# Kernel tuning notes

Hardware: AMD Instinct MI355X
Metric: run time of the kernel (lower is better)

## Reference

```python
import jax, jax.numpy as jnp
import numpy as np

ALPHA = 1.0  # softness coefficient


def _soft_assign(data, centroids):
    # data: (B, N, D), centroids: (B, K, D)
    # squared euclidean distance -> (B, N, K)
    dist = jnp.sum((data[:, :, None, :] - centroids[:, None, :, :]) ** 2, axis=-1)
    return jax.nn.softmax(-ALPHA * dist, axis=2)


def _update_once(data, probs):
    # weighted centroid update: (B, K, D)
    denom = jnp.sum(probs, axis=1)  # (B, K)
    centroids = jnp.einsum('bnk,bnd->bkd', probs, data) / denom[:, :, None]
    probs = _soft_assign(data, centroids)
    return probs, centroids


def setup_inputs() -> dict:
    key = jax.random.key(0)
    k1, k2 = jax.random.split(key)
    B, N, D, K = 8, 65536, 40, 2
    data = jax.random.normal(k1, (B, N, D), dtype=jnp.float32)
    centroid_ids = jax.random.randint(k2, (B, K), 0, N)
    return {"data": data, "centroid_ids": centroid_ids, "iteration": 10}


def reference(data, centroid_ids, iteration):
    # init centroids by gathering selected samples (random init path)
    centroids = jnp.take_along_axis(data, centroid_ids[:, :, None], axis=1)  # (B, K, D)
    probs = _soft_assign(data, centroids)

    def body(i, carry):
        probs, _ = carry
        return _update_once(data, probs)

    probs, centroids = jax.lax.fori_loop(0, iteration, body, (probs, centroids))
    return probs
```

## Files before the change

kernel.cpp:

```cpp
#include <hip/hip_runtime.h>
#include <hip/hip_fp16.h>
#include <cstddef>

#define BB    8
#define NN    65536
#define DD    40
#define NITER 10

#define PREPB  128
#define PTPB   256
#define PTILES 2
#define PSTR   21
#define PBLK   64
#define TPB    256
#define PPT    4
#define ROW    44



__device__ __forceinline__ float rfl(float x) {
    return __int_as_float(__builtin_amdgcn_readfirstlane(__float_as_int(x)));
}
__device__ __forceinline__ float prob0(float diff) {
    return __builtin_amdgcn_rcpf(1.f + __expf(diff));
}
__device__ __forceinline__ float2 h2f(unsigned u) {
    return __half22float2(*(const __half2*)&u);
}

__device__ __forceinline__ void gh_from_ids(const float* __restrict__ data,
                                            const int* __restrict__ ids, int b,
                                            float gs[DD], float& hs, int tid) {
    __shared__ float gbuf[DD], sqbuf[DD], hbuf;
    if (tid < DD) {
        const int i0 = ids[b * 2 + 0];
        const int i1 = ids[b * 2 + 1];
        const float c0 = data[((size_t)b * NN + i0) * DD + tid];
        const float c1 = data[((size_t)b * NN + i1) * DD + tid];
        gbuf[tid]  = c0 - c1;
        sqbuf[tid] = c0 * c0 - c1 * c1;
    }
    __syncthreads();
    if (tid == 0) {
        float h = 0.f;
#pragma unroll
        for (int i = 0; i < DD; ++i) h += sqbuf[i];
        hbuf = h;
    }
    __syncthreads();
#pragma unroll
    for (int i = 0; i < DD; ++i) gs[i] = rfl(gbuf[i]);
    hs = rfl(hbuf);
    __syncthreads();
}

template <int ROWS>
__device__ __forceinline__ void gh_from_partials(const float* __restrict__ pp,
                                                 const float* __restrict__ S, int b,
                                                 float gs[DD], float& hs, int tid) {
    __shared__ float part[41][4];
    __shared__ float red[41], gbuf[DD], sqbuf[DD], hbuf;
    if (tid < 164) {
        const int v = tid % 41, q = tid / 41;
        const float* base = pp + (size_t)b * ROWS * ROW;
        float s = 0.f;
#pragma unroll 8
        for (int j = 0; j < ROWS / 4; ++j)
            s += base[(size_t)(q * (ROWS / 4) + j) * ROW + v];
        part[v][q] = s;
    }
    __syncthreads();
    if (tid < 41)
        red[tid] = (part[tid][0] + part[tid][1]) + (part[tid][2] + part[tid][3]);
    __syncthreads();
    if (tid < DD) {
        const float num = red[tid], den = red[DD];
        const float c0 = num / den;
        const float c1 = (S[b * DD + tid] - num) / ((float)NN - den);
        gbuf[tid]  = c0 - c1;
        sqbuf[tid] = c0 * c0 - c1 * c1;
    }
    __syncthreads();
    if (tid == 0) {
        float h = 0.f;
#pragma unroll
        for (int i = 0; i < DD; ++i) h += sqbuf[i];
        hbuf = h;
    }
    __syncthreads();
#pragma unroll
    for (int i = 0; i < DD; ++i) gs[i] = rfl(gbuf[i]);
    hs = rfl(hbuf);
    __syncthreads();
}


__global__ __launch_bounds__(PTPB, 3) void k_prep(const float* __restrict__ data,
                                                  const int* __restrict__ ids,
                                                  __half2* __restrict__ dataT,
                                                  float* __restrict__ psOut,
                                                  float* __restrict__ ppOut) {
    const int bid = blockIdx.x;
    const int b = bid & 7, pb = bid >> 3;
    const int tid = threadIdx.x;
    __shared__ unsigned stg[PTPB * PSTR];
    __half2* stgh = (__half2*)stg;

    float gs[DD], hs;
    gh_from_ids(data, ids, b, gs, hs, tid);

    float vals[2 * DD + 1];
#pragma unroll
    for (int i = 0; i <= 2 * DD; ++i) vals[i] = 0.f;

#pragma unroll
    for (int t = 0; t < PTILES; ++t) {
        const int basePt = pb * (PTPB * PTILES) + t * PTPB;
        const float4* src = (const float4*)(data + ((size_t)b * NN + basePt) * DD);
        __syncthreads();
#pragma unroll
        for (int j = 0; j < 10; ++j) {
            const unsigned f = tid + j * PTPB;
            const float4 v = src[f];
            const unsigned slot = (f / 10u) * PSTR + (f % 10u) * 2u;
            stgh[slot]     = __floats2half2_rn(v.x, v.y);
            stgh[slot + 1] = __floats2half2_rn(v.z, v.w);
        }
        __syncthreads();
        __half2 xh[20];
        const __half2* rp = stgh + tid * PSTR;
#pragma unroll
        for (int q = 0; q < 20; ++q) xh[q] = rp[q];

        __half2* dst = dataT + (size_t)b * (DD / 2) * NN + basePt + tid;
#pragma unroll
        for (int q = 0; q < 20; ++q) dst[(size_t)q * NN] = xh[q];

        float a0 = 0.f, a1 = 0.f, a2 = 0.f, a3 = 0.f;
#pragma unroll
        for (int q = 0; q < 20; ++q) {
            const float2 v = __half22float2(xh[q]);
            vals[41 + 2 * q] += v.x; vals[41 + 2 * q + 1] += v.y;
            if (q & 1) { a2 = fmaf(v.x, gs[2 * q], a2); a3 = fmaf(v.y, gs[2 * q + 1], a3); }
            else       { a0 = fmaf(v.x, gs[2 * q], a0); a1 = fmaf(v.y, gs[2 * q + 1], a1); }
        }
        const float p0 = prob0(fmaf(-2.f, (a0 + a1) + (a2 + a3), hs));
        vals[DD] += p0;
#pragma unroll
        for (int q = 0; q < 20; ++q) {
            const float2 v = __half22float2(xh[q]);
            vals[2 * q]     = fmaf(p0, v.x, vals[2 * q]);
            vals[2 * q + 1] = fmaf(p0, v.y, vals[2 * q + 1]);
        }
    }

#pragma unroll
    for (int i = 0; i <= 2 * DD; ++i) {
        vals[i] += __shfl_xor(vals[i], 32, 64);
        vals[i] += __shfl_xor(vals[i], 16, 64);
    }
    float* rbuf = (float*)stg;
    __shared__ float part2[2 * DD + 1][2];
    __syncthreads();
    const int lane = tid & 63, wave = tid >> 6;
    if (lane < 16) {
        const int row = wave * 16 + lane;
#pragma unroll
        for (int i = 0; i <= 2 * DD; ++i) rbuf[row * 84 + i] = vals[i];
    }
    __syncthreads();
    if (tid < 162) {
        const int v = tid % 81, q = tid / 81;
        float s = 0.f;
#pragma unroll 8
        for (int j = 0; j < 32; ++j) s += rbuf[(q * 32 + j) * 84 + v];
        part2[v][q] = s;
    }
    __syncthreads();
    if (tid < 81) {
        const float s = part2[tid][0] + part2[tid][1];
        if (tid < 41) ppOut[(size_t)(b * PREPB + pb) * ROW + tid] = s;
        else          psOut[(size_t)(b * PREPB + pb) * 40 + (tid - 41)] = s;
    }
}

__global__ void k_reduceS(const float* __restrict__ psIn, float* __restrict__ S) {
    const int tid = threadIdx.x;
    __shared__ float tmp[BB * DD][2];
    const int i = tid >> 1, half = tid & 1;
    if (i < BB * DD) {
        const int b = i / DD, d = i % DD;
        float s = 0.f;
#pragma unroll 8
        for (int r = 0; r < PREPB / 2; ++r)
            s += psIn[(size_t)(b * PREPB + half * (PREPB / 2) + r) * 40 + d];
        tmp[i][half] = s;
    }
    __syncthreads();
    if (i < BB * DD && half == 0) S[i] = tmp[i][0] + tmp[i][1];
}

template <int MODE, int ROWS>
__global__ __launch_bounds__(TPB, 2) void k_pass(const __half2* __restrict__ dataT,
                                                 const float* __restrict__ ppIn,
                                                 const float* __restrict__ S,
                                                 float* __restrict__ ppOut,
                                                 float* __restrict__ out) {
    const int bid = blockIdx.x;
    const int b = bid & 7, pb = bid >> 3;
    const int tid = threadIdx.x;

    float gs[DD], hs;
    gh_from_partials<ROWS>(ppIn, S, b, gs, hs, tid);

    const int n0 = pb * (TPB * PPT) + tid * PPT;
    const __half2* base = dataT + (size_t)b * (DD / 2) * NN + n0;

    unsigned xh0[20], xh1[20], xh2[20], xh3[20];
    float a00 = 0.f, a01 = 0.f, a10 = 0.f, a11 = 0.f;
    float a20 = 0.f, a21 = 0.f, a30 = 0.f, a31 = 0.f;
#pragma unroll
    for (int dp = 0; dp < DD / 2; ++dp) {
        const uint4 u = *(const uint4*)(base + (size_t)dp * NN);
        xh0[dp] = u.x; xh1[dp] = u.y; xh2[dp] = u.z; xh3[dp] = u.w;
        const float2 v0 = h2f(u.x), v1 = h2f(u.y), v2 = h2f(u.z), v3 = h2f(u.w);
        a00 = fmaf(v0.x, gs[2 * dp], a00); a01 = fmaf(v0.y, gs[2 * dp + 1], a01);
        a10 = fmaf(v1.x, gs[2 * dp], a10); a11 = fmaf(v1.y, gs[2 * dp + 1], a11);
        a20 = fmaf(v2.x, gs[2 * dp], a20); a21 = fmaf(v2.y, gs[2 * dp + 1], a21);
        a30 = fmaf(v3.x, gs[2 * dp], a30); a31 = fmaf(v3.y, gs[2 * dp + 1], a31);
    }
    const float p00 = prob0(fmaf(-2.f, a00 + a01, hs));
    const float p01 = prob0(fmaf(-2.f, a10 + a11, hs));
    const float p02 = prob0(fmaf(-2.f, a20 + a21, hs));
    const float p03 = prob0(fmaf(-2.f, a30 + a31, hs));

    if constexpr (MODE == 2) {
        float4* o = (float4*)(out + ((size_t)b * NN + n0) * 2);
        o[0] = make_float4(p00, 1.f - p00, p01, 1.f - p01);
        o[1] = make_float4(p02, 1.f - p02, p03, 1.f - p03);
    } else {
        float acc[DD + 1];
#pragma unroll
        for (int i = 0; i < DD; ++i) acc[i] = 0.f;
        acc[DD] = (p00 + p01) + (p02 + p03);
#pragma unroll
        for (int dp = 0; dp < DD / 2; ++dp) {
            const float2 v0 = h2f(xh0[dp]), v1 = h2f(xh1[dp]);
            const float2 v2 = h2f(xh2[dp]), v3 = h2f(xh3[dp]);
            acc[2 * dp]     = fmaf(p00, v0.x, fmaf(p01, v1.x,
                              fmaf(p02, v2.x, fmaf(p03, v3.x, acc[2 * dp]))));
            acc[2 * dp + 1] = fmaf(p00, v0.y, fmaf(p01, v1.y,
                              fmaf(p02, v2.y, fmaf(p03, v3.y, acc[2 * dp + 1]))));
        }

#pragma unroll
        for (int i = 0; i <= DD; ++i) {
            acc[i] += __shfl_xor(acc[i], 32, 64);
            acc[i] += __shfl_xor(acc[i], 16, 64);
        }
        __shared__ float rbuf[64 * ROW];
        __shared__ float part2[DD + 1][4];
        const int lane = tid & 63, wave = tid >> 6;
        if (lane < 16) {
            const int row = wave * 16 + lane;
#pragma unroll
            for (int i = 0; i <= DD; ++i) rbuf[row * ROW + i] = acc[i];
        }
        __syncthreads();
        if (tid < 164) {
            const int v = tid % 41, q = tid / 41;
            float s = 0.f;
#pragma unroll
            for (int j = 0; j < 16; ++j) s += rbuf[(q * 16 + j) * ROW + v];
            part2[v][q] = s;
        }
        __syncthreads();
        if (tid <= DD)
            ppOut[(size_t)(b * PBLK + pb) * ROW + tid] =
                (part2[tid][0] + part2[tid][1]) + (part2[tid][2] + part2[tid][3]);
    }
}


extern "C" void kernel_launch(void* const* d_in, const int* in_sizes, int n_in,
                              void* d_out, int out_size, void* d_ws, size_t ws_size,
                              hipStream_t stream) {
    const float* data = (const float*)d_in[0];
    const int*   ids  = (const int*)d_in[1];

    float* ws      = (float*)d_ws;
    __half2* dataT = (__half2*)ws;
    float* after   = ws + (size_t)BB * (DD / 2) * NN;
    float* pA      = after;
    float* pp1     = pA + (size_t)BB * PREPB * ROW;
    float* pp2     = pp1 + (size_t)BB * PBLK * ROW;
    float* pS      = pp2 + (size_t)BB * PBLK * ROW;
    float* S       = pS + (size_t)BB * PREPB * 40;
    float* out     = (float*)d_out;

    k_prep<<<PREPB * BB, PTPB, 0, stream>>>(data, ids, dataT, pS, pA);
    k_reduceS<<<1, 640, 0, stream>>>(pS, S);

    const int grid = PBLK * BB;
    k_pass<1, PREPB><<<grid, TPB, 0, stream>>>(dataT, pA, S, pp1, nullptr);
    const float* cur = pp1;
    float* nxt = pp2;
    for (int t = 0; t < NITER - 2; ++t) {
        k_pass<1, PBLK><<<grid, TPB, 0, stream>>>(dataT, cur, S, nxt, nullptr);
        const float* tmp = cur; cur = nxt; nxt = (float*)tmp;
    }
    k_pass<2, PBLK><<<grid, TPB, 0, stream>>>(dataT, cur, S, nullptr, out);
}
```

Before: 142.3 us.

## Fold column-sum reduction into first pass and prefetch data before centroid reduce

Removes the separate k_reduceS launch by having k_prep write per-block partials that include the per-dimension data sums. The first k_pass reduces these partials and stores S for later passes. Every pass now issues its half-precision data loads before the cross-block partial reduction, so the global load latency overlaps with the centroid computation. The cost is holding the 80 data registers live across the reduction and barriers, which may raise register pressure, and the first pass reads a wider partials buffer.

```diff
diff --git a/kernel.cpp b/kernel.cpp
--- a/kernel.cpp
+++ b/kernel.cpp
@@ -11,11 +11,11 @@
 #define PTPB   256
 #define PTILES 2
 #define PSTR   21
+#define ROW1   84
 #define PBLK   64
 #define TPB    256
 #define PPT    4
 #define ROW    44
-
 
 
 __device__ __forceinline__ float rfl(float x) {
@@ -54,19 +54,58 @@
     __syncthreads();
 }
 
-template <int ROWS>
-__device__ __forceinline__ void gh_from_partials(const float* __restrict__ pp,
-                                                 const float* __restrict__ S, int b,
-                                                 float gs[DD], float& hs, int tid) {
+__device__ __forceinline__ void gh_first(const float* __restrict__ pp,
+                                         float* __restrict__ Sg, int b,
+                                         float gs[DD], float& hs, int tid) {
+    __shared__ float part[81][2];
+    __shared__ float red[81], gbuf[DD], sqbuf[DD], hbuf;
+    if (tid < 162) {
+        const int v = tid % 81, q = tid / 81;
+        const float* base = pp + (size_t)b * PREPB * ROW1;
+        float s = 0.f;
+#pragma unroll 8
+        for (int j = 0; j < 64; ++j)
+            s += base[(size_t)(q * 64 + j) * ROW1 + v];
+        part[v][q] = s;
+    }
+    __syncthreads();
+    if (tid < 81) red[tid] = part[tid][0] + part[tid][1];
+    __syncthreads();
+    if (tid < DD) {
+        const float num = red[tid], den = red[DD];
+        const float Sd  = red[41 + tid];
+        Sg[b * DD + tid] = Sd;
+        const float c0 = num / den;
+        const float c1 = (Sd - num) / ((float)NN - den);
+        gbuf[tid]  = c0 - c1;
+        sqbuf[tid] = c0 * c0 - c1 * c1;
+    }
+    __syncthreads();
+    if (tid == 0) {
+        float h = 0.f;
+#pragma unroll
+        for (int i = 0; i < DD; ++i) h += sqbuf[i];
+        hbuf = h;
+    }
+    __syncthreads();
+#pragma unroll
+    for (int i = 0; i < DD; ++i) gs[i] = rfl(gbuf[i]);
+    hs = rfl(hbuf);
+    __syncthreads();
+}
+
+__device__ __forceinline__ void gh_iter(const float* __restrict__ pp,
+                                        const float* __restrict__ S, int b,
+                                        float gs[DD], float& hs, int tid) {
     __shared__ float part[41][4];
     __shared__ float red[41], gbuf[DD], sqbuf[DD], hbuf;
     if (tid < 164) {
         const int v = tid % 41, q = tid / 41;
-        const float* base = pp + (size_t)b * ROWS * ROW;
+        const float* base = pp + (size_t)b * PBLK * ROW;
         float s = 0.f;
 #pragma unroll 8
-        for (int j = 0; j < ROWS / 4; ++j)
-            s += base[(size_t)(q * (ROWS / 4) + j) * ROW + v];
+        for (int j = 0; j < 16; ++j)
+            s += base[(size_t)(q * 16 + j) * ROW + v];
         part[v][q] = s;
     }
     __syncthreads();
@@ -98,7 +137,6 @@
 __global__ __launch_bounds__(PTPB, 3) void k_prep(const float* __restrict__ data,
                                                   const int* __restrict__ ids,
                                                   __half2* __restrict__ dataT,
-                                                  float* __restrict__ psOut,
                                                   float* __restrict__ ppOut) {
     const int bid = blockIdx.x;
     const int b = bid & 7, pb = bid >> 3;
@@ -177,53 +215,39 @@
         part2[v][q] = s;
     }
     __syncthreads();
-    if (tid < 81) {
-        const float s = part2[tid][0] + part2[tid][1];
-        if (tid < 41) ppOut[(size_t)(b * PREPB + pb) * ROW + tid] = s;
-        else          psOut[(size_t)(b * PREPB + pb) * 40 + (tid - 41)] = s;
-    }
-}
-
-__global__ void k_reduceS(const float* __restrict__ psIn, float* __restrict__ S) {
-    const int tid = threadIdx.x;
-    __shared__ float tmp[BB * DD][2];
-    const int i = tid >> 1, half = tid & 1;
-    if (i < BB * DD) {
-        const int b = i / DD, d = i % DD;
-        float s = 0.f;
-#pragma unroll 8
-        for (int r = 0; r < PREPB / 2; ++r)
-            s += psIn[(size_t)(b * PREPB + half * (PREPB / 2) + r) * 40 + d];
-        tmp[i][half] = s;
-    }
-    __syncthreads();
-    if (i < BB * DD && half == 0) S[i] = tmp[i][0] + tmp[i][1];
-}
-
-template <int MODE, int ROWS>
+    if (tid < 81)
+        ppOut[(size_t)(b * PREPB + pb) * ROW1 + tid] = part2[tid][0] + part2[tid][1];
+}
+
+template <int MODE, int FIRST>
 __global__ __launch_bounds__(TPB, 2) void k_pass(const __half2* __restrict__ dataT,
                                                  const float* __restrict__ ppIn,
-                                                 const float* __restrict__ S,
+                                                 float* __restrict__ Sg,
                                                  float* __restrict__ ppOut,
                                                  float* __restrict__ out) {
     const int bid = blockIdx.x;
     const int b = bid & 7, pb = bid >> 3;
     const int tid = threadIdx.x;
 
+    const int n0 = pb * (TPB * PPT) + tid * PPT;
+    const __half2* basep = dataT + (size_t)b * (DD / 2) * NN + n0;
+    unsigned xh0[20], xh1[20], xh2[20], xh3[20];
+#pragma unroll
+    for (int dp = 0; dp < DD / 2; ++dp) {
+        const uint4 u = *(const uint4*)(basep + (size_t)dp * NN);
+        xh0[dp] = u.x; xh1[dp] = u.y; xh2[dp] = u.z; xh3[dp] = u.w;
+    }
+
     float gs[DD], hs;
-    gh_from_partials<ROWS>(ppIn, S, b, gs, hs, tid);
-
-    const int n0 = pb * (TPB * PPT) + tid * PPT;
-    const __half2* base = dataT + (size_t)b * (DD / 2) * NN + n0;
-
-    unsigned xh0[20], xh1[20], xh2[20], xh3[20];
+    if constexpr (FIRST) gh_first(ppIn, Sg, b, gs, hs, tid);
+    else                 gh_iter(ppIn, Sg, b, gs, hs, tid);
+
     float a00 = 0.f, a01 = 0.f, a10 = 0.f, a11 = 0.f;
     float a20 = 0.f, a21 = 0.f, a30 = 0.f, a31 = 0.f;
 #pragma unroll
     for (int dp = 0; dp < DD / 2; ++dp) {
-        const uint4 u = *(const uint4*)(base + (size_t)dp * NN);
-        xh0[dp] = u.x; xh1[dp] = u.y; xh2[dp] = u.z; xh3[dp] = u.w;
-        const float2 v0 = h2f(u.x), v1 = h2f(u.y), v2 = h2f(u.z), v3 = h2f(u.w);
+        const float2 v0 = h2f(xh0[dp]), v1 = h2f(xh1[dp]);
+        const float2 v2 = h2f(xh2[dp]), v3 = h2f(xh3[dp]);
         a00 = fmaf(v0.x, gs[2 * dp], a00); a01 = fmaf(v0.y, gs[2 * dp + 1], a01);
         a10 = fmaf(v1.x, gs[2 * dp], a10); a11 = fmaf(v1.y, gs[2 * dp + 1], a11);
         a20 = fmaf(v2.x, gs[2 * dp], a20); a21 = fmaf(v2.y, gs[2 * dp + 1], a21);
@@ -290,24 +314,21 @@
 
     float* ws      = (float*)d_ws;
     __half2* dataT = (__half2*)ws;
-    float* after   = ws + (size_t)BB * (DD / 2) * NN;
-    float* pA      = after;
-    float* pp1     = pA + (size_t)BB * PREPB * ROW;
+    float* pA      = ws + (size_t)BB * (DD / 2) * NN;
+    float* pp1     = pA + (size_t)BB * PREPB * ROW1;
     float* pp2     = pp1 + (size_t)BB * PBLK * ROW;
-    float* pS      = pp2 + (size_t)BB * PBLK * ROW;
-    float* S       = pS + (size_t)BB * PREPB * 40;
+    float* Sg      = pp2 + (size_t)BB * PBLK * ROW;
     float* out     = (float*)d_out;
 
-    k_prep<<<PREPB * BB, PTPB, 0, stream>>>(data, ids, dataT, pS, pA);
-    k_reduceS<<<1, 640, 0, stream>>>(pS, S);
+    k_prep<<<PREPB * BB, PTPB, 0, stream>>>(data, ids, dataT, pA);
 
     const int grid = PBLK * BB;
-    k_pass<1, PREPB><<<grid, TPB, 0, stream>>>(dataT, pA, S, pp1, nullptr);
+    k_pass<1, 1><<<grid, TPB, 0, stream>>>(dataT, pA, Sg, pp1, nullptr);
     const float* cur = pp1;
     float* nxt = pp2;
     for (int t = 0; t < NITER - 2; ++t) {
-        k_pass<1, PBLK><<<grid, TPB, 0, stream>>>(dataT, cur, S, nxt, nullptr);
+        k_pass<1, 0><<<grid, TPB, 0, stream>>>(dataT, cur, Sg, nxt, nullptr);
         const float* tmp = cur; cur = nxt; nxt = (float*)tmp;
     }
-    k_pass<2, PBLK><<<grid, TPB, 0, stream>>>(dataT, cur, S, nullptr, out);
-}
+    k_pass<2, 0><<<grid, TPB, 0, stream>>>(dataT, cur, Sg, nullptr, out);
+}
```

New measurement: 137.1 us, median of 2. -3.7%, faster.
